# Performance work log

Measured on AMD Instinct MI355X. Metric: run time of the kernel, lower is better.

## Reference

```python
import jax, jax.numpy as jnp
import numpy as np

N, E, F_IN, HID = 50000, 800000, 64, 64
RADIAL = 16  # 4 coordinate channels -> 4x4 gram matrix


def _l2norm(x, eps=1e-12):
    # F.normalize(x, dim=-1, p=2)
    n = jnp.linalg.norm(x, axis=-1, keepdims=True)
    return x / jnp.maximum(n, eps)


def setup_inputs() -> dict:
    key = jax.random.key(0)
    ks = jax.random.split(key, 14)

    def lin(k, i, o, scale=None):
        s = (1.0 / np.sqrt(i)) if scale is None else scale
        return (jax.random.normal(k, (i, o), jnp.float32) * s).astype(jnp.float32)

    return dict(
        h=jax.random.normal(ks[0], (N, F_IN), jnp.float32),
        Z=jax.random.normal(ks[1], (N, 4, 3), jnp.float32),
        row=jax.random.randint(ks[2], (E,), 0, N),
        col=jax.random.randint(ks[3], (E,), 0, N),
        # edge_mlp: Linear(2*F_IN+16, HID) -> ReLU -> Linear(HID, HID) -> ReLU
        We1=lin(ks[4], 2 * F_IN + RADIAL, HID), be1=jnp.zeros((HID,), jnp.float32),
        We2=lin(ks[5], HID, HID), be2=jnp.zeros((HID,), jnp.float32),
        # node_mlp: Linear(HID+F_IN+HID, HID) -> ReLU -> Linear(HID, F_IN)
        Wn1=lin(ks[6], HID + F_IN + HID, HID), bn1=jnp.zeros((HID,), jnp.float32),
        Wn2=lin(ks[7], HID, F_IN), bn2=jnp.zeros((F_IN,), jnp.float32),
        # coord_mlp: Linear(HID, HID) -> ReLU -> Linear(HID, 1, bias=False, xavier gain 1e-3)
        Wc1=lin(ks[8], HID, HID), bc1=jnp.zeros((HID,), jnp.float32),
        Wc2=lin(ks[9], HID, 1, scale=0.001),
        # coord_mlp_vel: Linear(F_IN, HID) -> ReLU -> Linear(HID, 1)
        Wv1=lin(ks[10], F_IN, HID), bv1=jnp.zeros((HID,), jnp.float32),
        Wv2=lin(ks[11], HID, 1), bv2=jnp.zeros((1,), jnp.float32),
    )


def reference(h, Z, row, col, We1, be1, We2, be2, Wn1, bn1, Wn2, bn2,
              Wc1, bc1, Wc2, Wv1, bv1, Wv2, bv2):
    n = h.shape[0]
    # ---- coord2radial ----
    coord_diff = Z[row] - Z[col]                                 # [E,4,3]
    gram = jnp.einsum('ejt,ekt->ejk', coord_diff, coord_diff)    # [E,4,4]
    radial = _l2norm(gram.reshape(gram.shape[0], -1))            # [E,16]
    # ---- edge model ----
    e_in = jnp.concatenate([h[row], h[col], radial], axis=1)     # [E,144]
    edge_feat = jax.nn.relu(jax.nn.relu(e_in @ We1 + be1) @ We2 + be2)  # [E,HID]
    # ---- coord model (segment-mean over receiving node `row`) ----
    phi = jax.nn.relu(edge_feat @ Wc1 + bc1) @ Wc2               # [E,1]
    trans = coord_diff * phi[:, :, None]                         # [E,4,3]
    seg = jax.ops.segment_sum(trans, row, num_segments=n)        # [N,4,3]
    ones_e = jnp.ones((row.shape[0],), trans.dtype)
    cnt_row = jnp.maximum(jax.ops.segment_sum(ones_e, row, num_segments=n), 1.0)
    f = seg / cnt_row[:, None, None]                             # coords_weight = 1.0
    Z_new = Z + f                                                # [N,4,3]
    # ---- node model ----
    agg = jax.ops.segment_sum(edge_feat, row, num_segments=n)    # [N,HID]
    cnt_col = jnp.maximum(jax.ops.segment_sum(ones_e, col, num_segments=n), 1.0)
    others = jax.ops.segment_sum(edge_feat, col, num_segments=n) / cnt_col[:, None]
    n_in = jnp.concatenate([others, h, agg], axis=1)             # [N, HID+F_IN+HID]
    h_new = h + (jax.nn.relu(n_in @ Wn1 + bn1) @ Wn2 + bn2)      # recurrent
    # ---- Isolated update: x = Z[:,0], v = Z[:,1], force = f[:,0] ----
    scale = jax.nn.relu(h_new @ Wv1 + bv1) @ Wv2 + bv2           # [N,1]
    v_new = scale * Z[:, 1] + f[:, 0]                            # [N,3]
    x_new = Z[:, 0] + v_new                                      # [N,3]
    return (h_new, Z_new, x_new, v_new)
```

## Files before the change

### kernel.cpp

```cpp
#include <hip/hip_runtime.h>
#include <stdint.h>


__device__ __forceinline__ uint32_t bf16round(float x) {
    uint32_t u = __float_as_uint(x);
    return (u + 0x7fffu + ((u >> 16) & 1u)) >> 16;
}
__device__ __forceinline__ uint32_t packbf(float a, float b) {
    return bf16round(a) | (bf16round(b) << 16);
}
__device__ __forceinline__ float bflo(uint32_t u) { return __uint_as_float(u << 16); }
__device__ __forceinline__ float bfhi(uint32_t u) { return __uint_as_float(u & 0xffff0000u); }
__device__ __forceinline__ float bfu(ushort u) { return __uint_as_float(((uint32_t)u) << 16); }

typedef __attribute__((ext_vector_type(8))) short short8;
typedef __attribute__((ext_vector_type(4))) float f32x4;

__device__ __forceinline__ int wave_incl_scan(int x) {
    int lane = threadIdx.x & 63;
    #pragma unroll
    for (int off = 1; off < 64; off <<= 1) {
        int y = __shfl_up(x, off, 64);
        if (lane >= off) x += y;
    }
    return x;
}

__global__ __launch_bounds__(256) void hist_rank(
    const int* __restrict__ row, const int* __restrict__ col,
    int* __restrict__ cntR, int* __restrict__ cntC,
    int* __restrict__ rank_r, int* __restrict__ rank_c, int E)
{
    int i = blockIdx.x * blockDim.x + threadIdx.x;
    int stride = gridDim.x * blockDim.x;
    for (; i < E; i += stride) {
        rank_r[i] = atomicAdd(&cntR[row[i]], 1);
        rank_c[i] = atomicAdd(&cntC[col[i]], 1);
    }
}

__global__ __launch_bounds__(1024) void scan_block(
    const int* __restrict__ srcR, const int* __restrict__ srcC,
    int* __restrict__ dstR, int* __restrict__ dstC,
    int* __restrict__ bsumR, int* __restrict__ bsumC, int N)
{
    const int* src = blockIdx.y ? srcC : srcR;
    int* dst  = blockIdx.y ? dstC : dstR;
    int* bsum = blockIdx.y ? bsumC : bsumR;
    __shared__ int s[17];
    int tid = threadIdx.x, lane = tid & 63, wid = tid >> 6;
    int i = blockIdx.x * 1024 + tid;
    int x = (i < N) ? src[i] : 0;
    int incl = wave_incl_scan(x);
    if (lane == 63) s[wid] = incl;
    __syncthreads();
    if (wid == 0) {
        int t = (lane < 16) ? s[lane] : 0;
        int sc = t;
        #pragma unroll
        for (int off = 1; off < 16; off <<= 1) {
            int y = __shfl_up(sc, off, 64);
            if (lane >= off) sc += y;
        }
        if (lane < 16) s[lane] = sc - t;
        if (lane == 15) s[16] = sc;
    }
    __syncthreads();
    if (i < N) dst[i] = s[wid] + incl - x;
    if (tid == 0) bsum[blockIdx.x] = s[16];
}

__global__ __launch_bounds__(64) void scan_totals(
    int* __restrict__ bsumR, int* __restrict__ bsumC,
    int* __restrict__ dstR, int* __restrict__ dstC, int nblk, int N)
{
    int lane = threadIdx.x;
    for (int which = 0; which < 2; which++) {
        int* bs = which ? bsumC : bsumR;
        int* dst = which ? dstC : dstR;
        int running = 0;
        for (int base = 0; base < nblk; base += 64) {
            int idx = base + lane;
            int x = (idx < nblk) ? bs[idx] : 0;
            int incl = wave_incl_scan(x);
            if (idx < nblk) bs[idx] = running + incl - x;
            running += __shfl(incl, 63, 64);
        }
        if (lane == 0) dst[N] = running;
    }
}

__global__ __launch_bounds__(1024) void scan_add(
    int* __restrict__ dstR, int* __restrict__ dstC,
    const int* __restrict__ bsumR, const int* __restrict__ bsumC, int N)
{
    int* dst = blockIdx.y ? dstC : dstR;
    const int* bsum = blockIdx.y ? bsumC : bsumR;
    int i = blockIdx.x * 1024 + threadIdx.x;
    if (i < N) dst[i] += bsum[blockIdx.x];
}

__global__ __launch_bounds__(256) void perm_build(
    const int* __restrict__ row, const int* __restrict__ col,
    const int* __restrict__ rowptr, const int* __restrict__ colptr,
    const int* __restrict__ rank_r, const int* __restrict__ rank_c,
    uint4* __restrict__ rs_pack, int E)
{
    int i = blockIdx.x * blockDim.x + threadIdx.x;
    int stride = gridDim.x * blockDim.x;
    for (; i < E; i += stride) {
        int r = row[i], c = col[i];
        int pr = rowptr[r] + rank_r[i];
        int pc = colptr[c] + rank_c[i];
        rs_pack[pr] = make_uint4((uint32_t)r, (uint32_t)c, (uint32_t)pc, 0u);
    }
}

__global__ __launch_bounds__(256) void precompute_xrowcol(
    const float* __restrict__ h, const float* __restrict__ We1,
    const float* __restrict__ be1,
    ushort* __restrict__ Xrow, ushort* __restrict__ Xcol,
    ushort* __restrict__ hbf, int N)
{
    __shared__ uint32_t sWa[32 * 64];
    __shared__ uint32_t sWb[32 * 64];
    __shared__ float sbe1[64];
    int tid = threadIdx.x;
    for (int idx = tid; idx < 32 * 64; idx += 256) {
        int p = idx >> 6, o = idx & 63;
        sWa[idx] = packbf(We1[(2 * p) * 64 + o],      We1[(2 * p + 1) * 64 + o]);
        sWb[idx] = packbf(We1[(64 + 2 * p) * 64 + o], We1[(64 + 2 * p + 1) * 64 + o]);
    }
    if (tid < 64) sbe1[tid] = be1[tid];
    __syncthreads();

    int lane = tid & 63;
    int wv = blockIdx.x * 4 + (tid >> 6);
    int nw = gridDim.x * 4;
    for (int n0 = wv; n0 < N; n0 += nw) {
        int n = __builtin_amdgcn_readfirstlane(n0);
        const float* hn = h + (size_t)n * 64;
        float acc1 = sbe1[lane], acc2 = 0.f;
        #pragma unroll 8
        for (int p = 0; p < 32; p++) {
            float a0 = hn[2 * p], a1 = hn[2 * p + 1];
            uint32_t wa = sWa[p * 64 + lane];
            uint32_t wb = sWb[p * 64 + lane];
            acc1 += a0 * bflo(wa) + a1 * bfhi(wa);
            acc2 += a0 * bflo(wb) + a1 * bfhi(wb);
        }
        Xrow[(size_t)n * 64 + lane] = (ushort)bf16round(acc1);
        Xcol[(size_t)n * 64 + lane] = (ushort)bf16round(acc2);
        hbf[(size_t)n * 64 + lane]  = (ushort)bf16round(hn[lane]);
    }
}

__global__ __launch_bounds__(256) void edge_kernel(
    const float* __restrict__ Z,
    const uint4* __restrict__ rs_pack,
    const ushort* __restrict__ Xrow, const ushort* __restrict__ Xcol,
    const float* __restrict__ We1, const float* __restrict__ We2, const float* __restrict__ be2,
    const float* __restrict__ Wc1, const float* __restrict__ bc1, const float* __restrict__ Wc2,
    ushort* __restrict__ ef_col,
    float* __restrict__ aggF, float* __restrict__ segF, int E)
{
    __shared__ ushort radT[4][16 * 32];
    __shared__ ushort h1T[4][16 * 72];
    __shared__ ushort efT[4][16 * 72];
    __shared__ ushort xrT[4][16 * 72];
    __shared__ float  cdT[4][16 * 12];
    __shared__ float  phiT[4][16];

    int tid   = threadIdx.x;
    int lane  = tid & 63;
    int wslot = tid >> 6;
    int l16   = lane & 15;
    int quad  = lane >> 4;

    short8 w1r[4], w2f0[4], w2f1[4], w3f0[4], w3f1[4];
    float be2v[4], bc1v[4], wc2v[4];
    #pragma unroll
    for (int nt = 0; nt < 4; nt++) {
        int n = nt * 16 + l16;
        #pragma unroll
        for (int j = 0; j < 8; j++) {
            int k = quad * 8 + j;
            w1r[nt][j]  = (k < 16) ? (short)bf16round(We1[(128 + k) * 64 + n]) : (short)0;
            w2f0[nt][j] = (short)bf16round(We2[k * 64 + n]);
            w2f1[nt][j] = (short)bf16round(We2[(32 + k) * 64 + n]);
            w3f0[nt][j] = (short)bf16round(Wc1[k * 64 + n]);
            w3f1[nt][j] = (short)bf16round(Wc1[(32 + k) * 64 + n]);
        }
        be2v[nt] = be2[n];
        bc1v[nt] = bc1[n];
        wc2v[nt] = Wc2[n];
    }

    {
        int e = lane >> 2, o = (lane & 3) * 4;
        *(uint2*)&radT[wslot][e * 32 + 16 + o] = make_uint2(0u, 0u);
    }

    int e_l = lane >> 2;
    int cb  = (lane & 3) * 3;

    const f32x4 z4 = {0.f, 0.f, 0.f, 0.f};
    int ntile = (E + 15) >> 4;
    for (int t = blockIdx.x * 4 + wslot; t < ntile; t += gridDim.x * 4) {
        int e0 = t * 16;
        int eidx = e0 + l16;
        int eclmp = min(eidx, E - 1);
        uint4 rsv = rs_pack[eclmp];
        int rowv = (int)rsv.x;
        int colv = (int)rsv.y;
        int pcv  = (int)rsv.z;

        {
            int off = lane & 7, es = lane >> 3;
            #pragma unroll
            for (int i = 0; i < 2; i++) {
                int e = es + i * 8;
                int nr = __shfl(rowv, e, 64);
                int nc = __shfl(colv, e, 64);
                uint4 vr = *(const uint4*)(Xrow + (size_t)nr * 64 + off * 8);
                uint4 vc = *(const uint4*)(Xcol + (size_t)nc * 64 + off * 8);
                *(uint4*)&xrT[wslot][e * 72 + off * 8] = vr;
                *(uint4*)&efT[wslot][e * 72 + off * 8] = vc;
            }
        }

        int rZ = __shfl(rowv, e_l, 64);
        int cZ = __shfl(colv, e_l, 64);
        const float* Zr = Z + (size_t)rZ * 12 + cb;
        const float* Zc = Z + (size_t)cZ * 12 + cb;
        float cd0 = Zr[0] - Zc[0];
        float cd1 = Zr[1] - Zc[1];
        float cd2 = Zr[2] - Zc[2];
        cdT[wslot][e_l * 12 + cb + 0] = cd0;
        cdT[wslot][e_l * 12 + cb + 1] = cd1;
        cdT[wslot][e_l * 12 + cb + 2] = cd2;

        int gbase = lane & ~3;
        float g0, g1, g2, g3;
        {
            float a0 = __shfl(cd0, gbase + 0, 64), b0 = __shfl(cd1, gbase + 0, 64), c0 = __shfl(cd2, gbase + 0, 64);
            float a1 = __shfl(cd0, gbase + 1, 64), b1 = __shfl(cd1, gbase + 1, 64), c1 = __shfl(cd2, gbase + 1, 64);
            float a2 = __shfl(cd0, gbase + 2, 64), b2 = __shfl(cd1, gbase + 2, 64), c2 = __shfl(cd2, gbase + 2, 64);
            float a3 = __shfl(cd0, gbase + 3, 64), b3 = __shfl(cd1, gbase + 3, 64), c3 = __shfl(cd2, gbase + 3, 64);
            g0 = cd0 * a0 + cd1 * b0 + cd2 * c0;
            g1 = cd0 * a1 + cd1 * b1 + cd2 * c1;
            g2 = cd0 * a2 + cd1 * b2 + cd2 * c2;
            g3 = cd0 * a3 + cd1 * b3 + cd2 * c3;
        }
        float s = g0 * g0 + g1 * g1 + g2 * g2 + g3 * g3;
        s += __shfl_xor(s, 1, 64);
        s += __shfl_xor(s, 2, 64);
        float inv = 1.f / fmaxf(sqrtf(s), 1e-12f);

        __builtin_amdgcn_wave_barrier();
        uint2 rp;
        rp.x = packbf(g0 * inv, g1 * inv);
        rp.y = packbf(g2 * inv, g3 * inv);
        *(uint2*)&radT[wslot][e_l * 32 + (lane & 3) * 4] = rp;
        __builtin_amdgcn_wave_barrier();

        short8 aR = *(const short8*)&radT[wslot][l16 * 32 + quad * 8];
        f32x4 c1t[4];
        #pragma unroll
        for (int nt = 0; nt < 4; nt++)
            c1t[nt] = __builtin_amdgcn_mfma_f32_16x16x32_bf16(aR, w1r[nt], z4, 0, 0, 0);

        __builtin_amdgcn_wave_barrier();
        #pragma unroll
        for (int nt = 0; nt < 4; nt++) {
            int n = nt * 16 + l16;
            #pragma unroll
            for (int reg = 0; reg < 4; reg++) {
                int eL = quad * 4 + reg;
                float hv = c1t[nt][reg]
                         + bfu(xrT[wslot][eL * 72 + n])
                         + bfu(efT[wslot][eL * 72 + n]);
                hv = fmaxf(hv, 0.f);
                h1T[wslot][eL * 72 + n] = (ushort)bf16round(hv);
            }
        }
        __builtin_amdgcn_wave_barrier();

        short8 a20 = *(const short8*)&h1T[wslot][l16 * 72 + quad * 8];
        short8 a21 = *(const short8*)&h1T[wslot][l16 * 72 + 32 + quad * 8];
        f32x4 c2t[4];
        #pragma unroll
        for (int nt = 0; nt < 4; nt++) {
            f32x4 a = __builtin_amdgcn_mfma_f32_16x16x32_bf16(a20, w2f0[nt], z4, 0, 0, 0);
            c2t[nt]  = __builtin_amdgcn_mfma_f32_16x16x32_bf16(a21, w2f1[nt], a, 0, 0, 0);
        }

        __builtin_amdgcn_wave_barrier();
        #pragma unroll
        for (int nt = 0; nt < 4; nt++) {
            int n = nt * 16 + l16;
            #pragma unroll
            for (int reg = 0; reg < 4; reg++) {
                float ef = fmaxf(c2t[nt][reg] + be2v[nt], 0.f);
                efT[wslot][(quad * 4 + reg) * 72 + n] = (ushort)bf16round(ef);
            }
        }
        __builtin_amdgcn_wave_barrier();

        {
            int off = lane & 7, es = lane >> 3;
            #pragma unroll
            for (int i = 0; i < 2; i++) {
                int e = es + i * 8;
                int pc = __shfl(pcv, e, 64);
                if (e0 + e < E)
                    *(uint4*)(ef_col + (size_t)pc * 64 + off * 8) =
                        *(const uint4*)&efT[wslot][e * 72 + off * 8];
            }
        }

        short8 a30 = *(const short8*)&efT[wslot][l16 * 72 + quad * 8];
        short8 a31 = *(const short8*)&efT[wslot][l16 * 72 + 32 + quad * 8];
        float ps[4] = {0.f, 0.f, 0.f, 0.f};
        #pragma unroll
        for (int nt = 0; nt < 4; nt++) {
            f32x4 a = __builtin_amdgcn_mfma_f32_16x16x32_bf16(a30, w3f0[nt], z4, 0, 0, 0);
            f32x4 c = __builtin_amdgcn_mfma_f32_16x16x32_bf16(a31, w3f1[nt], a, 0, 0, 0);
            #pragma unroll
            for (int reg = 0; reg < 4; reg++)
                ps[reg] += fmaxf(c[reg] + bc1v[nt], 0.f) * wc2v[nt];
        }
        #pragma unroll
        for (int reg = 0; reg < 4; reg++) {
            ps[reg] += __shfl_xor(ps[reg], 1, 64);
            ps[reg] += __shfl_xor(ps[reg], 2, 64);
            ps[reg] += __shfl_xor(ps[reg], 4, 64);
            ps[reg] += __shfl_xor(ps[reg], 8, 64);
        }
        __builtin_amdgcn_wave_barrier();
        if (l16 == 0) {
            f32x4 pv = {ps[0], ps[1], ps[2], ps[3]};
            *(f32x4*)&phiT[wslot][quad * 4] = pv;
        }
        __builtin_amdgcn_wave_barrier();

        {
            int curnode = __shfl(rowv, 0, 64);
            int a = 0;
            float accA = 0.f, accS = 0.f;
            #pragma unroll
            for (int e = 0; e < 16; e++) {
                bool valid = (e0 + e) < E;
                float v = valid ? bfu(efT[wslot][e * 72 + lane]) : 0.f;
                float sv = 0.f;
                if (lane < 12 && valid)
                    sv = phiT[wslot][e] * cdT[wslot][e * 12 + lane];
                accA += v;
                accS += sv;
                int nxt = (e < 15) ? __shfl(rowv, e + 1, 64) : -1;
                if (nxt != curnode) {
                    if (a > 0 && e < 15) {
                        aggF[(size_t)curnode * 64 + lane] = accA;
                        if (lane < 12) segF[(size_t)curnode * 12 + lane] = accS;
                    } else if ((e0 + a) < E) {
                        unsafeAtomicAdd(&aggF[(size_t)curnode * 64 + lane], accA);
                        if (lane < 12) unsafeAtomicAdd(&segF[(size_t)curnode * 12 + lane], accS);
                    }
                    curnode = nxt;
                    a = e + 1;
                    accA = 0.f;
                    accS = 0.f;
                }
            }
        }
        __builtin_amdgcn_wave_barrier();
    }
}

__global__ __launch_bounds__(256) void reduce_kernel(
    const int* __restrict__ colptr, const ushort* __restrict__ ef_col,
    ushort* __restrict__ othersB, int N)
{
    int tid = threadIdx.x;
    int lane = tid & 63, wslot = tid >> 6;
    int wv = blockIdx.x * 4 + wslot, nw = gridDim.x * 4;

    for (int n0 = wv; n0 < N; n0 += nw) {
        int n = __builtin_amdgcn_readfirstlane(n0);
        int cs = colptr[n], ceN = colptr[n + 1];
        float inv_col = 1.f / (float)max(ceN - cs, 1);

        float othv = 0.f;
        int p = cs;
        for (; p + 3 < ceN; p += 4) {
            float a = bfu(ef_col[(size_t)p * 64 + lane]);
            float b = bfu(ef_col[(size_t)(p + 1) * 64 + lane]);
            float c = bfu(ef_col[(size_t)(p + 2) * 64 + lane]);
            float d = bfu(ef_col[(size_t)(p + 3) * 64 + lane]);
            othv += (a + b) + (c + d);
        }
        for (; p < ceN; p++) othv += bfu(ef_col[(size_t)p * 64 + lane]);
        othv *= inv_col;

        othersB[(size_t)n * 64 + lane] = (ushort)bf16round(othv);
    }
}

__global__ __launch_bounds__(256) void mlp_kernel(
    const float* __restrict__ h, const float* __restrict__ Z,
    const ushort* __restrict__ hbf,
    const float* __restrict__ aggF, const ushort* __restrict__ othersB,
    const float* __restrict__ segF, const int* __restrict__ rowptr,
    const float* __restrict__ Wn1, const float* __restrict__ bn1,
    const float* __restrict__ Wn2, const float* __restrict__ bn2,
    const float* __restrict__ Wv1, const float* __restrict__ bv1,
    const float* __restrict__ Wv2, const float* __restrict__ bv2,
    float* __restrict__ out, int N)
{
    __shared__ ushort aT[4][16 * 200];
    __shared__ ushort h1T[4][16 * 72];
    __shared__ float  scT[4][16];
    __shared__ float  irT[4][16];

    int tid   = threadIdx.x;
    int lane  = tid & 63;
    int wslot = tid >> 6;
    int l16   = lane & 15;
    int quad  = lane >> 4;

    short8 wn1f[6][4], wn2f[2][4], wv1f[2][4];
    float bn1v[4], bn2v[4], bv1v[4], wv2v[4];
    #pragma unroll
    for (int nt = 0; nt < 4; nt++) {
        int n = nt * 16 + l16;
        #pragma unroll
        for (int kc = 0; kc < 6; kc++)
            #pragma unroll
            for (int j = 0; j < 8; j++)
                wn1f[kc][nt][j] = (short)bf16round(Wn1[(kc * 32 + quad * 8 + j) * 64 + n]);
        #pragma unroll
        for (int kc = 0; kc < 2; kc++)
            #pragma unroll
            for (int j = 0; j < 8; j++) {
                wn2f[kc][nt][j] = (short)bf16round(Wn2[(kc * 32 + quad * 8 + j) * 64 + n]);
                wv1f[kc][nt][j] = (short)bf16round(Wv1[(kc * 32 + quad * 8 + j) * 64 + n]);
            }
        bn1v[nt] = bn1[n];
        bn2v[nt] = bn2[n];
        bv1v[nt] = bv1[n];
        wv2v[nt] = Wv2[n];
    }
    float bv2s = bv2[0];

    const f32x4 z4 = {0.f, 0.f, 0.f, 0.f};
    size_t OZ = (size_t)N * 64, OX = (size_t)N * 76, OV = (size_t)N * 79;
    int ntile = (N + 15) >> 4;
    for (int t = blockIdx.x * 4 + wslot; t < ntile; t += gridDim.x * 4) {
        int n0 = t * 16;

        if (lane < 16) {
            int node = min(n0 + lane, N - 1);
            irT[wslot][lane] = 1.f / (float)max(rowptr[node + 1] - rowptr[node], 1);
        }

        {
            #pragma unroll
            for (int i = 0; i < 2; i++) {
                int c = i * 64 + lane;
                int r = c >> 3, off = c & 7;
                int nn = min(n0 + r, N - 1);
                uint4 vo = *(const uint4*)(othersB + (size_t)nn * 64 + off * 8);
                uint4 vh = *(const uint4*)(hbf     + (size_t)nn * 64 + off * 8);
                float4 f0 = *(const float4*)(aggF + (size_t)nn * 64 + off * 8);
                float4 f1 = *(const float4*)(aggF + (size_t)nn * 64 + off * 8 + 4);
                uint4 va = make_uint4(packbf(f0.x, f0.y), packbf(f0.z, f0.w),
                                      packbf(f1.x, f1.y), packbf(f1.z, f1.w));
                *(uint4*)&aT[wslot][r * 200 +       off * 8] = vo;
                *(uint4*)&aT[wslot][r * 200 +  64 + off * 8] = vh;
                *(uint4*)&aT[wslot][r * 200 + 128 + off * 8] = va;
            }
        }
        __builtin_amdgcn_wave_barrier();

        #pragma unroll
        for (int i = 0; i < 4; i++) {
            int nd = i * 4 + (lane >> 4);
            int comp = lane & 15;
            int node = n0 + nd;
            if (comp < 12 && node < N) {
                float f = segF[(size_t)node * 12 + comp] * irT[wslot][nd];
                out[OZ + (size_t)node * 12 + comp] = Z[(size_t)node * 12 + comp] + f;
            }
        }

        f32x4 c1t[4];
        short8 af[6];
        #pragma unroll
        for (int kc = 0; kc < 6; kc++)
            af[kc] = *(const short8*)&aT[wslot][l16 * 200 + kc * 32 + quad * 8];
        #pragma unroll
        for (int nt = 0; nt < 4; nt++) {
            f32x4 c = z4;
            #pragma unroll
            for (int kc = 0; kc < 6; kc++)
                c = __builtin_amdgcn_mfma_f32_16x16x32_bf16(af[kc], wn1f[kc][nt], c, 0, 0, 0);
            c1t[nt] = c;
        }
        __builtin_amdgcn_wave_barrier();
        #pragma unroll
        for (int nt = 0; nt < 4; nt++) {
            int n = nt * 16 + l16;
            #pragma unroll
            for (int reg = 0; reg < 4; reg++) {
                float hv = fmaxf(c1t[nt][reg] + bn1v[nt], 0.f);
                h1T[wslot][(quad * 4 + reg) * 72 + n] = (ushort)bf16round(hv);
            }
        }
        __builtin_amdgcn_wave_barrier();

        short8 a20 = *(const short8*)&h1T[wslot][l16 * 72 + quad * 8];
        short8 a21 = *(const short8*)&h1T[wslot][l16 * 72 + 32 + quad * 8];
        f32x4 hnewT[4];
        #pragma unroll
        for (int nt = 0; nt < 4; nt++) {
            f32x4 a = __builtin_amdgcn_mfma_f32_16x16x32_bf16(a20, wn2f[0][nt], z4, 0, 0, 0);
            f32x4 c = __builtin_amdgcn_mfma_f32_16x16x32_bf16(a21, wn2f[1][nt], a, 0, 0, 0);
            int n = nt * 16 + l16;
            #pragma unroll
            for (int reg = 0; reg < 4; reg++) {
                int node = n0 + quad * 4 + reg;
                int nc = min(node, N - 1);
                float hnew = h[(size_t)nc * 64 + n] + c[reg] + bn2v[nt];
                hnewT[nt][reg] = hnew;
                if (node < N) out[(size_t)node * 64 + n] = hnew;
            }
        }

        __builtin_amdgcn_wave_barrier();
        #pragma unroll
        for (int nt = 0; nt < 4; nt++) {
            int n = nt * 16 + l16;
            #pragma unroll
            for (int reg = 0; reg < 4; reg++)
                h1T[wslot][(quad * 4 + reg) * 72 + n] = (ushort)bf16round(hnewT[nt][reg]);
        }
        __builtin_amdgcn_wave_barrier();
        short8 a30 = *(const short8*)&h1T[wslot][l16 * 72 + quad * 8];
        short8 a31 = *(const short8*)&h1T[wslot][l16 * 72 + 32 + quad * 8];
        float ps[4] = {0.f, 0.f, 0.f, 0.f};
        #pragma unroll
        for (int nt = 0; nt < 4; nt++) {
            f32x4 a = __builtin_amdgcn_mfma_f32_16x16x32_bf16(a30, wv1f[0][nt], z4, 0, 0, 0);
            f32x4 c = __builtin_amdgcn_mfma_f32_16x16x32_bf16(a31, wv1f[1][nt], a, 0, 0, 0);
            #pragma unroll
            for (int reg = 0; reg < 4; reg++)
                ps[reg] += fmaxf(c[reg] + bv1v[nt], 0.f) * wv2v[nt];
        }
        #pragma unroll
        for (int reg = 0; reg < 4; reg++) {
            ps[reg] += __shfl_xor(ps[reg], 1, 64);
            ps[reg] += __shfl_xor(ps[reg], 2, 64);
            ps[reg] += __shfl_xor(ps[reg], 4, 64);
            ps[reg] += __shfl_xor(ps[reg], 8, 64);
        }
        __builtin_amdgcn_wave_barrier();
        if (l16 == 0) {
            f32x4 pv = {ps[0] + bv2s, ps[1] + bv2s, ps[2] + bv2s, ps[3] + bv2s};
            *(f32x4*)&scT[wslot][quad * 4] = pv;
        }
        __builtin_amdgcn_wave_barrier();

        if (lane < 48) {
            int nd = lane / 3, comp = lane - nd * 3;
            int node = n0 + nd;
            if (node < N) {
                float scale = scT[wslot][nd];
                float f = segF[(size_t)node * 12 + comp] * irT[wslot][nd];
                float v = scale * Z[(size_t)node * 12 + 3 + comp] + f;
                float x = Z[(size_t)node * 12 + comp] + v;
                out[OX + (size_t)node * 3 + comp] = x;
                out[OV + (size_t)node * 3 + comp] = v;
            }
        }
        __builtin_amdgcn_wave_barrier();
    }
}

extern "C" void kernel_launch(void* const* d_in, const int* in_sizes, int n_in,
                              void* d_out, int out_size, void* d_ws, size_t ws_size,
                              hipStream_t stream) {
    const float* h   = (const float*)d_in[0];
    const float* Z   = (const float*)d_in[1];
    const int*   row = (const int*)d_in[2];
    const int*   col = (const int*)d_in[3];
    const float* We1 = (const float*)d_in[4];
    const float* be1 = (const float*)d_in[5];
    const float* We2 = (const float*)d_in[6];
    const float* be2 = (const float*)d_in[7];
    const float* Wn1 = (const float*)d_in[8];
    const float* bn1 = (const float*)d_in[9];
    const float* Wn2 = (const float*)d_in[10];
    const float* bn2 = (const float*)d_in[11];
    const float* Wc1 = (const float*)d_in[12];
    const float* bc1 = (const float*)d_in[13];
    const float* Wc2 = (const float*)d_in[14];
    const float* Wv1 = (const float*)d_in[15];
    const float* bv1 = (const float*)d_in[16];
    const float* Wv2 = (const float*)d_in[17];
    const float* bv2 = (const float*)d_in[18];

    int N = in_sizes[0] / 64;
    int E = in_sizes[2];
    int nblk = (N + 1023) / 1024;

    char* ws = (char*)d_ws;
    size_t o = 0;
    int* cntR    = (int*)(ws + o); o += (size_t)N * 4;
    int* cntC    = (int*)(ws + o); o += (size_t)N * 4;
    float* aggF  = (float*)(ws + o); o += (size_t)N * 64 * 4;
    float* segF  = (float*)(ws + o); o += (size_t)N * 12 * 4;
    size_t zero_bytes = o;
    int* rowptr  = (int*)(ws + o); o += (size_t)(N + 1) * 4;
    int* colptr  = (int*)(ws + o); o += (size_t)(N + 1) * 4;
    int* bsumR   = (int*)(ws + o); o += (size_t)nblk * 4;
    int* bsumC   = (int*)(ws + o); o += (size_t)nblk * 4;
    int* rank_r  = (int*)(ws + o); o += (size_t)E * 4;
    int* rank_c  = (int*)(ws + o); o += (size_t)E * 4;
    o = (o + 15) & ~(size_t)15;
    uint4* rs_pack = (uint4*)(ws + o); o += (size_t)E * 16;
    ushort* Xrow = (ushort*)(ws + o); o += (size_t)N * 64 * 2;
    ushort* Xcol = (ushort*)(ws + o); o += (size_t)N * 64 * 2;
    ushort* hbf  = (ushort*)(ws + o); o += (size_t)N * 64 * 2;
    ushort* othersB = (ushort*)(ws + o); o += (size_t)N * 64 * 2;
    ushort* ef_col = (ushort*)(ws + o); o += (size_t)E * 64 * 2;
    float* out = (float*)d_out;

    hipMemsetAsync(d_ws, 0, zero_bytes, stream);
    hist_rank<<<1024, 256, 0, stream>>>(row, col, cntR, cntC, rank_r, rank_c, E);
    scan_block<<<dim3(nblk, 2), 1024, 0, stream>>>(cntR, cntC, rowptr, colptr,
                                                   bsumR, bsumC, N);
    scan_totals<<<1, 64, 0, stream>>>(bsumR, bsumC, rowptr, colptr, nblk, N);
    scan_add<<<dim3(nblk, 2), 1024, 0, stream>>>(rowptr, colptr, bsumR, bsumC, N);
    perm_build<<<1024, 256, 0, stream>>>(row, col, rowptr, colptr,
                                         rank_r, rank_c, rs_pack, E);
    precompute_xrowcol<<<512, 256, 0, stream>>>(h, We1, be1, Xrow, Xcol, hbf, N);
    edge_kernel<<<1024, 256, 0, stream>>>(Z, rs_pack, Xrow, Xcol,
                                          We1, We2, be2, Wc1, bc1, Wc2,
                                          ef_col, aggF, segF, E);
    reduce_kernel<<<2048, 256, 0, stream>>>(colptr, ef_col, othersB, N);
    mlp_kernel<<<800, 256, 0, stream>>>(h, Z, hbf, aggF, othersB, segF, rowptr,
                                        Wn1, bn1, Wn2, bn2, Wv1, bv1, Wv2, bv2,
                                        out, N);
}
```

Baseline: 463.6 us.

## Prefetch edge indices, build radial MFMA operand via shuffles, ballot segment boundaries

```diff
diff --git a/kernel.cpp b/kernel.cpp
--- a/kernel.cpp
+++ b/kernel.cpp
@@ -164,7 +164,6 @@
     ushort* __restrict__ ef_col,
     float* __restrict__ aggF, float* __restrict__ segF, int E)
 {
-    __shared__ ushort radT[4][16 * 32];
     __shared__ ushort h1T[4][16 * 72];
     __shared__ ushort efT[4][16 * 72];
     __shared__ ushort xrT[4][16 * 72];
@@ -196,24 +195,26 @@
         wc2v[nt] = Wc2[n];
     }
 
-    {
-        int e = lane >> 2, o = (lane & 3) * 4;
-        *(uint2*)&radT[wslot][e * 32 + 16 + o] = make_uint2(0u, 0u);
-    }
-
     int e_l = lane >> 2;
     int cb  = (lane & 3) * 3;
 
     const f32x4 z4 = {0.f, 0.f, 0.f, 0.f};
     int ntile = (E + 15) >> 4;
-    for (int t = blockIdx.x * 4 + wslot; t < ntile; t += gridDim.x * 4) {
+    int stride = gridDim.x * 4;
+    int t = blockIdx.x * 4 + wslot;
+
+    uint4 rsv = make_uint4(0u, 0u, 0u, 0u);
+    if (t < ntile) rsv = rs_pack[min(t * 16 + l16, E - 1)];
+
+    for (; t < ntile; t += stride) {
         int e0 = t * 16;
-        int eidx = e0 + l16;
-        int eclmp = min(eidx, E - 1);
-        uint4 rsv = rs_pack[eclmp];
-        int rowv = (int)rsv.x;
-        int colv = (int)rsv.y;
-        int pcv  = (int)rsv.z;
+        uint4 rsc = rsv;
+        int tn = t + stride;
+        if (tn < ntile) rsv = rs_pack[min(tn * 16 + l16, E - 1)];
+
+        int rowv = (int)rsc.x;
+        int colv = (int)rsc.y;
+        int pcv  = (int)rsc.z;
 
         {
             int off = lane & 7, es = lane >> 3;
@@ -257,14 +258,23 @@
         s += __shfl_xor(s, 2, 64);
         float inv = 1.f / fmaxf(sqrtf(s), 1e-12f);
 
-        __builtin_amdgcn_wave_barrier();
-        uint2 rp;
-        rp.x = packbf(g0 * inv, g1 * inv);
-        rp.y = packbf(g2 * inv, g3 * inv);
-        *(uint2*)&radT[wslot][e_l * 32 + (lane & 3) * 4] = rp;
-        __builtin_amdgcn_wave_barrier();
-
-        short8 aR = *(const short8*)&radT[wslot][l16 * 32 + quad * 8];
+        uint32_t rpx = packbf(g0 * inv, g1 * inv);
+        uint32_t rpy = packbf(g2 * inv, g3 * inv);
+
+        short8 aR;
+        {
+            int s0 = l16 * 4 + quad * 2;
+            uint32_t x0 = __shfl(rpx, s0, 64), y0 = __shfl(rpy, s0, 64);
+            uint32_t x1 = __shfl(rpx, s0 + 1, 64), y1 = __shfl(rpy, s0 + 1, 64);
+            union { short8 v; uint32_t u[4]; } au;
+            bool qlo = (quad < 2);
+            au.u[0] = qlo ? x0 : 0u;
+            au.u[1] = qlo ? y0 : 0u;
+            au.u[2] = qlo ? x1 : 0u;
+            au.u[3] = qlo ? y1 : 0u;
+            aR = au.v;
+        }
+
         f32x4 c1t[4];
         #pragma unroll
         for (int nt = 0; nt < 4; nt++)
@@ -345,28 +355,31 @@
         __builtin_amdgcn_wave_barrier();
 
         {
-            int curnode = __shfl(rowv, 0, 64);
+            int rnext = __shfl_down(rowv, 1, 64);
+            unsigned long long bl = __ballot(rowv != rnext);
+            uint32_t mask = (uint32_t)bl & 0x7FFFu;
+
+            float accA = 0.f, accS = 0.f;
             int a = 0;
-            float accA = 0.f, accS = 0.f;
             #pragma unroll
             for (int e = 0; e < 16; e++) {
                 bool valid = (e0 + e) < E;
                 float v = valid ? bfu(efT[wslot][e * 72 + lane]) : 0.f;
-                float sv = 0.f;
+                accA += v;
                 if (lane < 12 && valid)
-                    sv = phiT[wslot][e] * cdT[wslot][e * 12 + lane];
-                accA += v;
-                accS += sv;
-                int nxt = (e < 15) ? __shfl(rowv, e + 1, 64) : -1;
-                if (nxt != curnode) {
-                    if (a > 0 && e < 15) {
-                        aggF[(size_t)curnode * 64 + lane] = accA;
-                        if (lane < 12) segF[(size_t)curnode * 12 + lane] = accS;
-                    } else if ((e0 + a) < E) {
-                        unsafeAtomicAdd(&aggF[(size_t)curnode * 64 + lane], accA);
-                        if (lane < 12) unsafeAtomicAdd(&segF[(size_t)curnode * 12 + lane], accS);
+                    accS += phiT[wslot][e] * cdT[wslot][e * 12 + lane];
+                if (e == 15 || ((mask >> e) & 1u)) {
+                    int node = __shfl(rowv, e, 64);
+                    bool interior = (a > 0) && (e < 15);
+                    if ((e0 + a) < E) {
+                        if (interior) {
+                            aggF[(size_t)node * 64 + lane] = accA;
+                            if (lane < 12) segF[(size_t)node * 12 + lane] = accS;
+                        } else {
+                            unsafeAtomicAdd(&aggF[(size_t)node * 64 + lane], accA);
+                            if (lane < 12) unsafeAtomicAdd(&segF[(size_t)node * 12 + lane], accS);
+                        }
                     }
-                    curnode = nxt;
                     a = e + 1;
                     accA = 0.f;
                     accS = 0.f;
@@ -644,7 +657,7 @@
     perm_build<<<1024, 256, 0, stream>>>(row, col, rowptr, colptr,
                                          rank_r, rank_c, rs_pack, E);
     precompute_xrowcol<<<512, 256, 0, stream>>>(h, We1, be1, Xrow, Xcol, hbf, N);
-    edge_kernel<<<1024, 256, 0, stream>>>(Z, rs_pack, Xrow, Xcol,
+    edge_kernel<<<1280, 256, 0, stream>>>(Z, rs_pack, Xrow, Xcol,
                                           We1, We2, be2, Wc1, bc1, Wc2,
                                           ef_col, aggF, segF, E);
     reduce_kernel<<<2048, 256, 0, stream>>>(colptr, ef_col, othersB, N);
```

Result: slower. 544.2 us (+17.4%).
